# Kernel optimization log

Hardware: AMD Instinct MI355X
Metric: run time of the kernel (lower is better)

## Reference

```python
import jax, jax.numpy as jnp
import numpy as np

B, TT, C, H, T = 4, 4096, 1024, 16, 128
K = C // H  # head size (rk and v head sizes equal here)
HEAD_DIV = 8.0  # head_size_divisor
EPS = 1e-5  # GroupNorm eps
LAYER_ID, N_LAYER = 12, 24


def setup_inputs() -> dict:
    key = jax.random.key(0)
    ks = jax.random.split(key, 8)
    r01 = LAYER_ID / (N_LAYER - 1)
    r1a0 = 1.0 - LAYER_ID / N_LAYER
    ddd = (jnp.arange(C, dtype=jnp.float32) / C).reshape(1, 1, C)
    h = jnp.arange(H, dtype=jnp.float32)
    scale = 0.02
    return {
        "xq": jax.random.normal(ks[0], (B, TT, C), jnp.float32),
        "time_mix_k": ddd ** r1a0,
        "time_mix_v": ddd ** r1a0 + 0.3 * r01,
        "time_mix_r": ddd ** (0.5 * r1a0),
        "time_mix_g": ddd ** (0.5 * r1a0),
        "time_decay": -8.0 + 7.0 * (h / (H - 1)) ** (0.7 + 1.3 * r01),
        "time_faaaa": r01 * (1.0 - h / (H - 1)),
        "W_r": jax.random.normal(ks[1], (C, C), jnp.float32) * scale,
        "W_k": jax.random.normal(ks[2], (C, C), jnp.float32) * scale,
        "W_v": jax.random.normal(ks[3], (C, C), jnp.float32) * scale,
        "W_g": jax.random.normal(ks[4], (C, C), jnp.float32) * scale,
        "W_o": jax.random.normal(ks[5], (C, C), jnp.float32) * scale,
        "ln_w": jnp.ones((C,), jnp.float32),
        "ln_b": jnp.zeros((C,), jnp.float32),
    }


def reference(xq, time_mix_k, time_mix_v, time_mix_r, time_mix_g,
              time_decay, time_faaaa, W_r, W_k, W_v, W_g, W_o, ln_w, ln_b):
    x = xq
    B_, TT_, C_ = x.shape
    N = TT_ // T  # number of chunks
    # time shift: xx[:, t] = x[:, t-1], xx[:, 0] = 0
    xx = jnp.pad(x, ((0, 0), (1, 0), (0, 0)))[:, :-1]
    xr = x * time_mix_r + xx * (1 - time_mix_r)
    xk = x * time_mix_k + xx * (1 - time_mix_k)
    xv = x * time_mix_v + xx * (1 - time_mix_v)
    xg = x * time_mix_g + xx * (1 - time_mix_g)
    r = (xr @ W_r.T).reshape(B_, TT_, H, K).transpose(0, 2, 1, 3)  # (B,H,TT,K)
    k = (xk @ W_k.T).reshape(B_, TT_, H, K).transpose(0, 2, 1, 3)
    v = (xv @ W_v.T).reshape(B_, TT_, H, K).transpose(0, 2, 1, 3)
    g = jax.nn.silu(xg @ W_g.T)  # (B,TT,C)

    decay = jnp.exp(-jnp.exp(time_decay))  # (H,)
    u = time_faaaa  # (H,)
    ws = decay ** T  # per-chunk state decay (H,)
    i_idx = jnp.arange(T)
    wb = decay[:, None] ** i_idx                # (H,T): decay^i
    wk = decay[:, None] ** (T - 1 - i_idx)      # (H,T): decay^(T-1-j)
    diff = i_idx[:, None] - i_idx[None, :]      # i - j
    pw = decay[:, None, None] ** jnp.maximum(diff - 1, 0)
    # lower-triangular intra-chunk decay: decay^(i-j-1) for i>j, u on diag
    w_mat = jnp.where(diff > 0, pw, 0.0) + jnp.eye(T, dtype=x.dtype) * u[:, None, None]  # (H,T,T)

    # chunked layout: (N, B, H, T, K)
    rc = r.reshape(B_, H, N, T, K).transpose(2, 0, 1, 3, 4)
    kc = k.reshape(B_, H, N, T, K).transpose(2, 0, 1, 3, 4)
    vc = v.reshape(B_, H, N, T, K).transpose(2, 0, 1, 3, 4)
    s0 = jnp.zeros((B_, H, K, K), x.dtype)

    def step(s, chunk):
        rr, kk, vv = chunk
        att = jnp.einsum('bhik,bhjk->bhij', rr, kk) * w_mat
        out = att @ vv + jnp.einsum('bhik,bhkv->bhiv', rr, s) * wb[None, :, :, None]
        s_new = ws[None, :, None, None] * s + jnp.einsum(
            'bhjk,bhjv->bhkv', kk * wk[None, :, :, None], vv)
        return s_new, out

    _, xo = jax.lax.scan(step, s0, (rc, kc, vc))  # xo: (N,B,H,T,K)
    xo = xo.transpose(1, 0, 3, 2, 4).reshape(B_, TT_, H, K)

    # GroupNorm(H groups) over channels, applied to x / head_size_divisor
    y = xo / HEAD_DIV
    mu = y.mean(-1, keepdims=True)
    var = y.var(-1, keepdims=True)
    y = (y - mu) / jnp.sqrt(var + EPS)
    y = y * ln_w.reshape(H, K) + ln_b.reshape(H, K)
    y = y.reshape(B_, TT_, C_)
    return (y * g) @ W_o.T
```

## Files before the change

### kernel.cpp

```cpp
#include <hip/hip_runtime.h>
#include <hip/hip_bf16.h>
#include <stdint.h>

#define C_DIM 1024
#define H_DIM 16
#define K_DIM 64
#define T_CH 128
#define TT_DIM 4096
#define B_DIM 4
#define N_CH 32
#define M_ROWS 16384

typedef __attribute__((ext_vector_type(8))) __bf16 bf16x8;
typedef __attribute__((ext_vector_type(4))) float floatx4;

__device__ __forceinline__ float bf2f(ushort u) {
  union { uint32_t i; float f; } v; v.i = ((uint32_t)u) << 16; return v.f;
}
__device__ __forceinline__ ushort f2bf(float f) {
  union { float f; uint32_t i; } v; v.f = f;
  return (ushort)((v.i + 0x7fffu + ((v.i >> 16) & 1u)) >> 16);
}

#define GLOAD_LDS16(g, l)                                                     \
  __builtin_amdgcn_global_load_lds(                                           \
      (const __attribute__((address_space(1))) void*)(g),                     \
      (__attribute__((address_space(3))) void*)(l), 16, 0, 0)

__global__ __launch_bounds__(256) void mix_kernel(
    const float* __restrict__ x,
    const float* __restrict__ mk, const float* __restrict__ mv,
    const float* __restrict__ mr, const float* __restrict__ mg,
    ushort* __restrict__ xr, ushort* __restrict__ xk,
    ushort* __restrict__ xv, ushort* __restrict__ xg) {
  long idx = (long)blockIdx.x * 256 + threadIdx.x;
  long e = idx * 4;
  int c = (int)(e & (C_DIM - 1));
  long row = e >> 10;
  int t = (int)(row & (TT_DIM - 1));
  floatx4 xc = *(const floatx4*)(x + e);
  floatx4 xp = {0.f, 0.f, 0.f, 0.f};
  if (t != 0) xp = *(const floatx4*)(x + e - C_DIM);
  floatx4 d = xc - xp;
  floatx4 vk = *(const floatx4*)(mk + c);
  floatx4 vv = *(const floatx4*)(mv + c);
  floatx4 vr = *(const floatx4*)(mr + c);
  floatx4 vg = *(const floatx4*)(mg + c);
  floatx4 ok = xp + d * vk;
  floatx4 ov = xp + d * vv;
  floatx4 orr = xp + d * vr;
  floatx4 og = xp + d * vg;
  union { ushort u[4]; uint2 q; } pk;
#define ST(dst, val)                                                          \
  pk.u[0] = f2bf(val.x); pk.u[1] = f2bf(val.y);                               \
  pk.u[2] = f2bf(val.z); pk.u[3] = f2bf(val.w);                               \
  *(uint2*)((dst) + e) = pk.q;
  ST(xk, ok) ST(xv, ov) ST(xr, orr) ST(xg, og)
#undef ST
}

__global__ __launch_bounds__(256) void wconv_kernel(
    const float* __restrict__ w0, const float* __restrict__ w1,
    const float* __restrict__ w2, const float* __restrict__ w3,
    const float* __restrict__ w4, ushort* __restrict__ o) {
  long idx = (long)blockIdx.x * 256 + threadIdx.x;
  long e = idx * 4;
  int wi = (int)(e >> 20);
  long off = e & ((1L << 20) - 1);
  const float* src = wi == 0 ? w0 : wi == 1 ? w1 : wi == 2 ? w2 : wi == 3 ? w3 : w4;
  floatx4 vv = *(const floatx4*)(src + off);
  union { ushort u[4]; uint2 q; } pk;
  pk.u[0] = f2bf(vv.x); pk.u[1] = f2bf(vv.y);
  pk.u[2] = f2bf(vv.z); pk.u[3] = f2bf(vv.w);
  *(uint2*)(o + e) = pk.q;
}

#define BARX() __builtin_amdgcn_s_barrier()
#define VMW4() asm volatile("s_waitcnt vmcnt(4)" ::: "memory")
#define VMW0() asm volatile("s_waitcnt vmcnt(0)" ::: "memory")
#define LGKW() asm volatile("s_waitcnt lgkmcnt(0)" ::: "memory")

template <int EPI>
__global__ __launch_bounds__(512, 2) void gemm_bt(
    const ushort* __restrict__ A, const ushort* __restrict__ Bt,
    void* __restrict__ Cout) {
  __shared__ __align__(16) ushort smem[65536];
  const int tid = threadIdx.x;
  const int lane = tid & 63, w = tid >> 6;
  const int q = lane >> 4, l16 = lane & 15;
  const int wm = w >> 2, wn = w & 3;
  const int id = blockIdx.x;
  const int wg = (id & 7) * 32 + (id >> 3);
  const int bm = wg >> 2, bn = wg & 3;

  const int r8 = tid >> 3;
  const int c8 = ((tid & 7) ^ (r8 & 7)) * 8;
  const ushort* gA = A + (long)(bm * 256 + r8) * C_DIM + c8;
  const ushort* gB = Bt + (long)(bn * 256 + r8) * C_DIM + c8;

  const char* sB = (const char*)smem;
  const int arow = (wm * 128 + l16) * 128;
  const int brow = (wn * 64 + l16) * 128;
  const int swz = (l16 & 7) << 4;
  const int csv[2] = {(q << 4) ^ swz, ((4 + q) << 4) ^ swz};

  floatx4 acc[8][4] = {};
  bf16x8 af[4][2];
  bf16x8 bfv[4][2];

#define STAGE(ISA, sl, hh, tile)                                              \
  do {                                                                        \
    const ushort* g_ = (ISA ? gA : gB) + ((hh) * 131072 + (tile) * 64);       \
    ushort* l_ = smem + ((ISA ? 0 : 32768) + (sl) * 16384 + (hh) * 8192 +     \
                         w * 512);                                            \
    GLOAD_LDS16(g_, l_);                         \
    GLOAD_LDS16(g_ + 65536, l_ + 4096);                \
  } while (0)

#define READ_A(sl, qr)                                                        \
  do {                                                                        \
    _Pragma("unroll") for (int i_ = 0; i_ < 4; ++i_) {                        \
      af[i_][0] = *(const bf16x8*)(sB + (sl) * 32768 + arow + (qr) * 8192 +   \
                                   i_ * 2048 + csv[0]);                       \
      af[i_][1] = *(const bf16x8*)(sB + (sl) * 32768 + arow + (qr) * 8192 +   \
                                   i_ * 2048 + csv[1]);                       \
    }                                                                         \
  } while (0)

#define READ_B(sl, qc)                                                        \
  do {                                                                        \
    _Pragma("unroll") for (int j_ = 0; j_ < 2; ++j_) {                        \
      bfv[(qc) * 2 + j_][0] = *(const bf16x8*)(sB + 65536 + (sl) * 32768 +    \
                                               brow + (qc) * 4096 +           \
                                               j_ * 2048 + csv[0]);           \
      bfv[(qc) * 2 + j_][1] = *(const bf16x8*)(sB + 65536 + (sl) * 32768 +    \
                                               brow + (qc) * 4096 +           \
                                               j_ * 2048 + csv[1]);           \
    }                                                                         \
  } while (0)

#define MFMA_Q(qr, qc)                                                        \
  do {                                                                        \
    __builtin_amdgcn_s_setprio(1);                                            \
    _Pragma("unroll") for (int i_ = 0; i_ < 4; ++i_)                          \
        _Pragma("unroll") for (int j_ = 0; j_ < 2; ++j_) {                    \
      acc[(qr) * 4 + i_][(qc) * 2 + j_] =                                     \
          __builtin_amdgcn_mfma_f32_16x16x32_bf16(                            \
              af[i_][0], bfv[(qc) * 2 + j_][0],                               \
              acc[(qr) * 4 + i_][(qc) * 2 + j_], 0, 0, 0);                    \
      acc[(qr) * 4 + i_][(qc) * 2 + j_] =                                     \
          __builtin_amdgcn_mfma_f32_16x16x32_bf16(                            \
              af[i_][1], bfv[(qc) * 2 + j_][1],                               \
              acc[(qr) * 4 + i_][(qc) * 2 + j_], 0, 0, 0);                    \
    }                                                                         \
    __builtin_amdgcn_s_setprio(0);                                            \
  } while (0)

  STAGE(1, 0, 0, 0); STAGE(1, 0, 1, 0);
  STAGE(0, 0, 0, 0); STAGE(0, 0, 1, 0);
  STAGE(0, 1, 0, 1); STAGE(0, 1, 1, 1);
  VMW4();
  BARX();

#pragma unroll 1
  for (int i = 0; i < 7; ++i) {
    const int t1 = 2 * i + 1, tn0 = 2 * i + 2, tn1 = 2 * i + 3;
    READ_A(0, 0); READ_B(0, 0); STAGE(1, 1, 0, t1);
    BARX(); MFMA_Q(0, 0); LGKW(); BARX();
    READ_B(0, 1); STAGE(1, 1, 1, t1);
    BARX(); MFMA_Q(0, 1); LGKW(); BARX();
    READ_A(0, 1); STAGE(0, 0, 0, tn0);
    BARX(); MFMA_Q(1, 0); LGKW(); BARX();
    STAGE(0, 0, 1, tn0); VMW4();
    BARX(); MFMA_Q(1, 1); LGKW(); BARX();
    READ_A(1, 0); READ_B(1, 0); STAGE(1, 0, 0, tn0);
    BARX(); MFMA_Q(0, 0); LGKW(); BARX();
    READ_B(1, 1); STAGE(1, 0, 1, tn0);
    BARX(); MFMA_Q(0, 1); LGKW(); BARX();
    READ_A(1, 1); STAGE(0, 1, 0, tn1);
    BARX(); MFMA_Q(1, 0); LGKW(); BARX();
    STAGE(0, 1, 1, tn1); VMW4();
    BARX(); MFMA_Q(1, 1); LGKW(); BARX();
  }
  READ_A(0, 0); READ_B(0, 0); STAGE(1, 1, 0, 15);
  BARX(); MFMA_Q(0, 0); LGKW(); BARX();
  READ_B(0, 1); STAGE(1, 1, 1, 15);
  BARX(); MFMA_Q(0, 1); LGKW(); BARX();
  READ_A(0, 1);
  BARX(); MFMA_Q(1, 0); LGKW(); BARX();
  VMW0();
  BARX(); MFMA_Q(1, 1); LGKW(); BARX();
  READ_A(1, 0); READ_B(1, 0);
  BARX(); MFMA_Q(0, 0); LGKW(); BARX();
  READ_B(1, 1);
  BARX(); MFMA_Q(0, 1); LGKW(); BARX();
  READ_A(1, 1);
  BARX(); MFMA_Q(1, 0); LGKW(); BARX();
  BARX(); MFMA_Q(1, 1);

  const int row0 = bm * 256 + wm * 128 + q * 4;
  const int col0 = bn * 256 + wn * 64 + l16;
#pragma unroll
  for (int fi = 0; fi < 8; ++fi)
#pragma unroll
    for (int fj = 0; fj < 4; ++fj)
#pragma unroll
      for (int rg = 0; rg < 4; ++rg) {
        long off = (long)(row0 + fi * 16 + rg) * C_DIM + col0 + fj * 16;
        float val = acc[fi][fj][rg];
        if (EPI == 1) val = val / (1.f + expf(-val));
        if (EPI == 2)
          ((float*)Cout)[off] = val;
        else
          ((ushort*)Cout)[off] = f2bf(val);
      }
#undef STAGE
#undef READ_A
#undef READ_B
#undef MFMA_Q
}

__global__ __launch_bounds__(256) void chunk_state(
    const ushort* __restrict__ kB, const ushort* __restrict__ vB,
    const float* __restrict__ td, ushort* __restrict__ Zc) {
  __shared__ __align__(16) ushort vt_s[64 * 136];
  __shared__ __align__(16) ushort kwt_s[64 * 136];
  int blk = blockIdx.x;
  int bh = blk >> 5, n = blk & 31;
  int b = bh >> 4, h = bh & 15;
  int tid = threadIdx.x;
  int lane = tid & 63, w = tid >> 6;
  int q = lane >> 4, l16 = lane & 15;
  float etd = expf(td[h]);
  long cbase = ((long)b * TT_DIM + n * T_CH) * C_DIM + h * K_DIM;

#pragma unroll
  for (int it = 0; it < 4; it++) {
    int chunk = it * 256 + tid;
    int row = chunk >> 3;
    int cc = (chunk & 7) * 8;
    long ga = cbase + (long)row * C_DIM + cc;
    uint4 kv4 = *(const uint4*)(kB + ga);
    uint4 vv4 = *(const uint4*)(vB + ga);
    float wkj = expf(-(float)(T_CH - 1 - row) * etd);
    const ushort* kp = (const ushort*)&kv4;
    const ushort* vp = (const ushort*)&vv4;
#pragma unroll
    for (int e2 = 0; e2 < 8; e2++) {
      kwt_s[(cc + e2) * 136 + row] = f2bf(bf2f(kp[e2]) * wkj);
      vt_s[(cc + e2) * 136 + row] = vp[e2];
    }
  }
  __syncthreads();

  floatx4 accZ[4] = {};
#pragma unroll
  for (int js = 0; js < 128; js += 32) {
    bf16x8 av = *(const bf16x8*)&vt_s[(w * 16 + l16) * 136 + q * 8 + js];
    bf16x8 bk3[4];
#pragma unroll
    for (int kt = 0; kt < 4; kt++)
      bk3[kt] = *(const bf16x8*)&kwt_s[(kt * 16 + l16) * 136 + q * 8 + js];
#pragma unroll
    for (int kt = 0; kt < 4; kt++)
      accZ[kt] = __builtin_amdgcn_mfma_f32_16x16x32_bf16(av, bk3[kt], accZ[kt], 0, 0, 0);
  }
  long zbase = (long)blk * 4096;
#pragma unroll
  for (int kt = 0; kt < 4; kt++)
#pragma unroll
    for (int rg = 0; rg < 4; rg++)
      Zc[zbase + (w * 16 + q * 4 + rg) * 64 + kt * 16 + l16] = f2bf(accZ[kt][rg]);
}

__global__ __launch_bounds__(256) void state_scan(
    const ushort* __restrict__ Zc, const float* __restrict__ td,
    ushort* __restrict__ Sb) {
  long tg = (long)blockIdx.x * 256 + threadIdx.x;
  int bh = (int)(tg >> 12);
  int e = (int)(tg & 4095);
  int h = bh & 15;
  float wsf = expf(-128.f * expf(td[h]));
  float s = 0.f;
  long base = (long)bh * N_CH * 4096 + e;
#pragma unroll
  for (int n = 0; n < N_CH; n++) {
    Sb[base + n * 4096] = f2bf(s);
    s = wsf * s + bf2f(Zc[base + n * 4096]);
  }
}

__global__ __launch_bounds__(256) void chunk_out(
    const ushort* __restrict__ rB, const ushort* __restrict__ kB,
    const ushort* __restrict__ vB, const ushort* __restrict__ gBuf,
    const ushort* __restrict__ Sb,
    const float* __restrict__ td, const float* __restrict__ tf,
    const float* __restrict__ lnw, const float* __restrict__ lnb,
    ushort* __restrict__ gy) {
  __shared__ __align__(16) ushort rr_s[128 * 72];
  __shared__ __align__(16) ushort un_s[128 * 136];
  __shared__ __align__(16) ushort vt_s[64 * 136];
  __shared__ __align__(16) ushort z_s[64 * 72];

  int blk = blockIdx.x;
  int bh = blk >> 5, n = blk & 31;
  int b = bh >> 4, h = bh & 15;
  int tid = threadIdx.x;
  int lane = tid & 63, w = tid >> 6;
  int q = lane >> 4, l16 = lane & 15;

  float etd = expf(td[h]);
  float u = tf[h];
  long cbase = ((long)b * TT_DIM + n * T_CH) * C_DIM + h * K_DIM;

#pragma unroll
  for (int it = 0; it < 4; it++) {
    int chunk = it * 256 + tid;
    int row = chunk >> 3;
    int cc = (chunk & 7) * 8;
    long ga = cbase + (long)row * C_DIM + cc;
    *(uint4*)&rr_s[row * 72 + cc] = *(const uint4*)(rB + ga);
    *(uint4*)&un_s[row * 136 + cc] = *(const uint4*)(kB + ga);
    uint4 vv4 = *(const uint4*)(vB + ga);
    const ushort* vp = (const ushort*)&vv4;
#pragma unroll
    for (int e2 = 0; e2 < 8; e2++) vt_s[(cc + e2) * 136 + row] = vp[e2];
  }
  {
    long sbase = (long)blk * 4096;
    int v = tid >> 2, c0 = (tid & 3) * 16;
    *(uint4*)&z_s[v * 72 + c0] = *(const uint4*)(Sb + sbase + v * 64 + c0);
    *(uint4*)&z_s[v * 72 + c0 + 8] = *(const uint4*)(Sb + sbase + v * 64 + c0 + 8);
  }
  __syncthreads();

  floatx4 accA[4][4] = {};
  int ai0 = (w >> 1) * 64, aj0 = (w & 1) * 64;
#pragma unroll
  for (int ks = 0; ks < 64; ks += 32) {
    bf16x8 af[4], bk2[4];
#pragma unroll
    for (int i = 0; i < 4; i++)
      af[i] = *(const bf16x8*)&rr_s[(ai0 + i * 16 + l16) * 72 + q * 8 + ks];
#pragma unroll
    for (int j = 0; j < 4; j++)
      bk2[j] = *(const bf16x8*)&un_s[(aj0 + j * 16 + l16) * 136 + q * 8 + ks];
#pragma unroll
    for (int mi = 0; mi < 4; mi++)
#pragma unroll
      for (int nj = 0; nj < 4; nj++)
        accA[mi][nj] = __builtin_amdgcn_mfma_f32_16x16x32_bf16(
            af[mi], bk2[nj], accA[mi][nj], 0, 0, 0);
  }

  floatx4 accB[2][4] = {};
  int i0 = w * 32;
#pragma unroll
  for (int ks = 0; ks < 64; ks += 32) {
    bf16x8 af2[2], bz[4];
#pragma unroll
    for (int it2 = 0; it2 < 2; it2++)
      af2[it2] = *(const bf16x8*)&rr_s[(i0 + it2 * 16 + l16) * 72 + q * 8 + ks];
#pragma unroll
    for (int vt2 = 0; vt2 < 4; vt2++)
      bz[vt2] = *(const bf16x8*)&z_s[(vt2 * 16 + l16) * 72 + q * 8 + ks];
#pragma unroll
    for (int it2 = 0; it2 < 2; it2++)
#pragma unroll
      for (int vt2 = 0; vt2 < 4; vt2++)
        accB[it2][vt2] = __builtin_amdgcn_mfma_f32_16x16x32_bf16(
            af2[it2], bz[vt2], accB[it2][vt2], 0, 0, 0);
  }
  __syncthreads();

#pragma unroll
  for (int mi = 0; mi < 4; mi++)
#pragma unroll
    for (int nj = 0; nj < 4; nj++)
#pragma unroll
      for (int rg = 0; rg < 4; rg++) {
        int i = ai0 + mi * 16 + q * 4 + rg;
        int j = aj0 + nj * 16 + l16;
        float wv = 0.f;
        if (i > j) wv = expf(-(float)(i - j - 1) * etd);
        else if (i == j) wv = u;
        un_s[i * 136 + j] = f2bf(accA[mi][nj][rg] * wv);
      }
  __syncthreads();

  floatx4 accO[2][4] = {};
#pragma unroll
  for (int js = 0; js < 128; js += 32) {
    bf16x8 af3[2], bv[4];
#pragma unroll
    for (int it2 = 0; it2 < 2; it2++)
      af3[it2] = *(const bf16x8*)&un_s[(i0 + it2 * 16 + l16) * 136 + q * 8 + js];
#pragma unroll
    for (int vt2 = 0; vt2 < 4; vt2++)
      bv[vt2] = *(const bf16x8*)&vt_s[(vt2 * 16 + l16) * 136 + q * 8 + js];
#pragma unroll
    for (int it2 = 0; it2 < 2; it2++)
#pragma unroll
      for (int vt2 = 0; vt2 < 4; vt2++)
        accO[it2][vt2] = __builtin_amdgcn_mfma_f32_16x16x32_bf16(
            af3[it2], bv[vt2], accO[it2][vt2], 0, 0, 0);
  }

#pragma unroll
  for (int it2 = 0; it2 < 2; it2++)
#pragma unroll
    for (int rg = 0; rg < 4; rg++) {
      int i = i0 + it2 * 16 + q * 4 + rg;
      float wbi = expf(-(float)i * etd);
      float vals[4];
      float s1 = 0.f, s2 = 0.f;
#pragma unroll
      for (int vt2 = 0; vt2 < 4; vt2++) {
        float val = accO[it2][vt2][rg] + wbi * accB[it2][vt2][rg];
        vals[vt2] = val; s1 += val; s2 += val * val;
      }
#pragma unroll
      for (int mm = 1; mm < 16; mm <<= 1) {
        s1 += __shfl_xor(s1, mm, 64);
        s2 += __shfl_xor(s2, mm, 64);
      }
      float mu = s1 * (1.f / 64.f);
      float va = s2 * (1.f / 64.f) - mu * mu;
      float rinv = rsqrtf(va + 64.f * 1e-5f);
      long rowg = (long)b * TT_DIM + n * T_CH + i;
#pragma unroll
      for (int vt2 = 0; vt2 < 4; vt2++) {
        int c = h * K_DIM + vt2 * 16 + l16;
        float y = (vals[vt2] - mu) * rinv * lnw[c] + lnb[c];
        float gf = bf2f(gBuf[rowg * C_DIM + c]);
        gy[rowg * C_DIM + c] = f2bf(y * gf);
      }
    }
}

extern "C" void kernel_launch(void* const* d_in, const int* in_sizes, int n_in,
                              void* d_out, int out_size, void* d_ws,
                              size_t ws_size, hipStream_t stream) {
  const float* xq  = (const float*)d_in[0];
  const float* tmk = (const float*)d_in[1];
  const float* tmv = (const float*)d_in[2];
  const float* tmr = (const float*)d_in[3];
  const float* tmg = (const float*)d_in[4];
  const float* td  = (const float*)d_in[5];
  const float* tf  = (const float*)d_in[6];
  const float* Wr  = (const float*)d_in[7];
  const float* Wk  = (const float*)d_in[8];
  const float* Wv  = (const float*)d_in[9];
  const float* Wg  = (const float*)d_in[10];
  const float* Wo  = (const float*)d_in[11];
  const float* lnw = (const float*)d_in[12];
  const float* lnb = (const float*)d_in[13];

  char* ws = (char*)d_ws;
  const size_t BUF = (size_t)M_ROWS * C_DIM * 2;
  ushort* b0 = (ushort*)(ws + 0 * BUF);
  ushort* b1 = (ushort*)(ws + 1 * BUF);
  ushort* b2 = (ushort*)(ws + 2 * BUF);
  ushort* b3 = (ushort*)(ws + 3 * BUF);
  ushort* wcv = (ushort*)(ws + 4 * BUF);
  const ushort* wr_b = wcv;
  const ushort* wk_b = wcv + (1 << 20);
  const ushort* wv_b = wcv + 2 * (1 << 20);
  const ushort* wg_b = wcv + 3 * (1 << 20);
  const ushort* wo_b = wcv + 4 * (1 << 20);
  ushort* Zc = (ushort*)(ws + 4 * BUF + 5 * (2 << 20));
  ushort* Sb = Zc + (size_t)64 * N_CH * 4096;
  ushort* rbuf = (ushort*)d_out;

  mix_kernel<<<16384, 256, 0, stream>>>(xq, tmk, tmv, tmr, tmg, b0, b1, b2, b3);
  wconv_kernel<<<5120, 256, 0, stream>>>(Wr, Wk, Wv, Wg, Wo, wcv);

  gemm_bt<0><<<256, 512, 0, stream>>>(b0, wr_b, rbuf);
  gemm_bt<0><<<256, 512, 0, stream>>>(b1, wk_b, b0);
  gemm_bt<0><<<256, 512, 0, stream>>>(b2, wv_b, b1);
  gemm_bt<1><<<256, 512, 0, stream>>>(b3, wg_b, b2);

  chunk_state<<<2048, 256, 0, stream>>>(b0, b1, td, Zc);
  state_scan<<<1024, 256, 0, stream>>>(Zc, td, Sb);
  chunk_out<<<2048, 256, 0, stream>>>(rbuf, b0, b1, b2, Sb, td, tf, lnw, lnb, b3);

  gemm_bt<2><<<256, 512, 0, stream>>>(b3, wo_b, (float*)d_out);
}
```

Before: 434.9 us.

## Swizzle transposed LDS tiles and widen chunk_out to 512 threads

```diff
diff --git a/kernel.cpp b/kernel.cpp
--- a/kernel.cpp
+++ b/kernel.cpp
@@ -113,8 +113,8 @@
     const ushort* g_ = (ISA ? gA : gB) + ((hh) * 131072 + (tile) * 64);       \
     ushort* l_ = smem + ((ISA ? 0 : 32768) + (sl) * 16384 + (hh) * 8192 +     \
                          w * 512);                                            \
-    GLOAD_LDS16(g_, l_);                         \
-    GLOAD_LDS16(g_ + 65536, l_ + 4096);                \
+    GLOAD_LDS16(g_, l_);                                                      \
+    GLOAD_LDS16(g_ + 65536, l_ + 4096);                                       \
   } while (0)
 
 #define READ_A(sl, qr)                                                        \
@@ -245,10 +245,13 @@
     float wkj = expf(-(float)(T_CH - 1 - row) * etd);
     const ushort* kp = (const ushort*)&kv4;
     const ushort* vp = (const ushort*)&vv4;
+    int cb2 = row >> 3;
 #pragma unroll
     for (int e2 = 0; e2 < 8; e2++) {
-      kwt_s[(cc + e2) * 136 + row] = f2bf(bf2f(kp[e2]) * wkj);
-      vt_s[(cc + e2) * 136 + row] = vp[e2];
+      int vr = cc + e2;
+      int ph = vr * 136 + ((cb2 ^ ((vr >> 3) & 7)) << 3) + (row & 7);
+      kwt_s[ph] = f2bf(bf2f(kp[e2]) * wkj);
+      vt_s[ph] = vp[e2];
     }
   }
   __syncthreads();
@@ -256,11 +259,15 @@
   floatx4 accZ[4] = {};
 #pragma unroll
   for (int js = 0; js < 128; js += 32) {
-    bf16x8 av = *(const bf16x8*)&vt_s[(w * 16 + l16) * 136 + q * 8 + js];
+    int cb = q + (js >> 3);
+    int vrA = w * 16 + l16;
+    bf16x8 av = *(const bf16x8*)&vt_s[vrA * 136 + ((cb ^ ((vrA >> 3) & 7)) << 3)];
     bf16x8 bk3[4];
 #pragma unroll
-    for (int kt = 0; kt < 4; kt++)
-      bk3[kt] = *(const bf16x8*)&kwt_s[(kt * 16 + l16) * 136 + q * 8 + js];
+    for (int kt = 0; kt < 4; kt++) {
+      int vrB = kt * 16 + l16;
+      bk3[kt] = *(const bf16x8*)&kwt_s[vrB * 136 + ((cb ^ ((vrB >> 3) & 7)) << 3)];
+    }
 #pragma unroll
     for (int kt = 0; kt < 4; kt++)
       accZ[kt] = __builtin_amdgcn_mfma_f32_16x16x32_bf16(av, bk3[kt], accZ[kt], 0, 0, 0);
@@ -290,7 +297,7 @@
   }
 }
 
-__global__ __launch_bounds__(256) void chunk_out(
+__global__ __launch_bounds__(512, 4) void chunk_out(
     const ushort* __restrict__ rB, const ushort* __restrict__ kB,
     const ushort* __restrict__ vB, const ushort* __restrict__ gBuf,
     const ushort* __restrict__ Sb,
@@ -301,6 +308,7 @@
   __shared__ __align__(16) ushort un_s[128 * 136];
   __shared__ __align__(16) ushort vt_s[64 * 136];
   __shared__ __align__(16) ushort z_s[64 * 72];
+  __shared__ float pw_s[128];
 
   int blk = blockIdx.x;
   int bh = blk >> 5, n = blk & 31;
@@ -313,9 +321,11 @@
   float u = tf[h];
   long cbase = ((long)b * TT_DIM + n * T_CH) * C_DIM + h * K_DIM;
 
-#pragma unroll
-  for (int it = 0; it < 4; it++) {
-    int chunk = it * 256 + tid;
+  if (tid < 128) pw_s[tid] = expf(-(float)tid * etd);
+
+#pragma unroll
+  for (int it = 0; it < 2; it++) {
+    int chunk = it * 512 + tid;
     int row = chunk >> 3;
     int cc = (chunk & 7) * 8;
     long ga = cbase + (long)row * C_DIM + cc;
@@ -323,119 +333,115 @@
     *(uint4*)&un_s[row * 136 + cc] = *(const uint4*)(kB + ga);
     uint4 vv4 = *(const uint4*)(vB + ga);
     const ushort* vp = (const ushort*)&vv4;
-#pragma unroll
-    for (int e2 = 0; e2 < 8; e2++) vt_s[(cc + e2) * 136 + row] = vp[e2];
+    int cb2 = row >> 3;
+#pragma unroll
+    for (int e2 = 0; e2 < 8; e2++) {
+      int vr = cc + e2;
+      vt_s[vr * 136 + ((cb2 ^ ((vr >> 3) & 7)) << 3) + (row & 7)] = vp[e2];
+    }
   }
   {
     long sbase = (long)blk * 4096;
-    int v = tid >> 2, c0 = (tid & 3) * 16;
+    int v = tid >> 3, c0 = (tid & 7) * 8;
     *(uint4*)&z_s[v * 72 + c0] = *(const uint4*)(Sb + sbase + v * 64 + c0);
-    *(uint4*)&z_s[v * 72 + c0 + 8] = *(const uint4*)(Sb + sbase + v * 64 + c0 + 8);
   }
   __syncthreads();
 
-  floatx4 accA[4][4] = {};
-  int ai0 = (w >> 1) * 64, aj0 = (w & 1) * 64;
+  int ar0 = (w >> 1) * 32, ac0 = (w & 1) * 64;
+  floatx4 accA[2][4] = {};
 #pragma unroll
   for (int ks = 0; ks < 64; ks += 32) {
-    bf16x8 af[4], bk2[4];
-#pragma unroll
-    for (int i = 0; i < 4; i++)
-      af[i] = *(const bf16x8*)&rr_s[(ai0 + i * 16 + l16) * 72 + q * 8 + ks];
+    bf16x8 af[2], bk2[4];
+#pragma unroll
+    for (int i = 0; i < 2; i++)
+      af[i] = *(const bf16x8*)&rr_s[(ar0 + i * 16 + l16) * 72 + q * 8 + ks];
 #pragma unroll
     for (int j = 0; j < 4; j++)
-      bk2[j] = *(const bf16x8*)&un_s[(aj0 + j * 16 + l16) * 136 + q * 8 + ks];
-#pragma unroll
-    for (int mi = 0; mi < 4; mi++)
+      bk2[j] = *(const bf16x8*)&un_s[(ac0 + j * 16 + l16) * 136 + q * 8 + ks];
+#pragma unroll
+    for (int mi = 0; mi < 2; mi++)
 #pragma unroll
       for (int nj = 0; nj < 4; nj++)
         accA[mi][nj] = __builtin_amdgcn_mfma_f32_16x16x32_bf16(
             af[mi], bk2[nj], accA[mi][nj], 0, 0, 0);
   }
 
-  floatx4 accB[2][4] = {};
-  int i0 = w * 32;
+  int i0 = w * 16;
+  floatx4 accB[4] = {};
 #pragma unroll
   for (int ks = 0; ks < 64; ks += 32) {
-    bf16x8 af2[2], bz[4];
-#pragma unroll
-    for (int it2 = 0; it2 < 2; it2++)
-      af2[it2] = *(const bf16x8*)&rr_s[(i0 + it2 * 16 + l16) * 72 + q * 8 + ks];
+    bf16x8 af2 = *(const bf16x8*)&rr_s[(i0 + l16) * 72 + q * 8 + ks];
+    bf16x8 bz[4];
 #pragma unroll
     for (int vt2 = 0; vt2 < 4; vt2++)
       bz[vt2] = *(const bf16x8*)&z_s[(vt2 * 16 + l16) * 72 + q * 8 + ks];
 #pragma unroll
-    for (int it2 = 0; it2 < 2; it2++)
-#pragma unroll
-      for (int vt2 = 0; vt2 < 4; vt2++)
-        accB[it2][vt2] = __builtin_amdgcn_mfma_f32_16x16x32_bf16(
-            af2[it2], bz[vt2], accB[it2][vt2], 0, 0, 0);
+    for (int vt2 = 0; vt2 < 4; vt2++)
+      accB[vt2] = __builtin_amdgcn_mfma_f32_16x16x32_bf16(
+          af2, bz[vt2], accB[vt2], 0, 0, 0);
   }
   __syncthreads();
 
 #pragma unroll
-  for (int mi = 0; mi < 4; mi++)
+  for (int mi = 0; mi < 2; mi++)
 #pragma unroll
     for (int nj = 0; nj < 4; nj++)
 #pragma unroll
       for (int rg = 0; rg < 4; rg++) {
-        int i = ai0 + mi * 16 + q * 4 + rg;
-        int j = aj0 + nj * 16 + l16;
+        int i = ar0 + mi * 16 + q * 4 + rg;
+        int j = ac0 + nj * 16 + l16;
         float wv = 0.f;
-        if (i > j) wv = expf(-(float)(i - j - 1) * etd);
+        if (i > j) wv = pw_s[i - j - 1];
         else if (i == j) wv = u;
         un_s[i * 136 + j] = f2bf(accA[mi][nj][rg] * wv);
       }
   __syncthreads();
 
-  floatx4 accO[2][4] = {};
+  floatx4 accO[4] = {};
 #pragma unroll
   for (int js = 0; js < 128; js += 32) {
-    bf16x8 af3[2], bv[4];
-#pragma unroll
-    for (int it2 = 0; it2 < 2; it2++)
-      af3[it2] = *(const bf16x8*)&un_s[(i0 + it2 * 16 + l16) * 136 + q * 8 + js];
+    bf16x8 af3 = *(const bf16x8*)&un_s[(i0 + l16) * 136 + q * 8 + js];
+    int cb = q + (js >> 3);
+    bf16x8 bv[4];
+#pragma unroll
+    for (int vt2 = 0; vt2 < 4; vt2++) {
+      int vr = vt2 * 16 + l16;
+      bv[vt2] = *(const bf16x8*)&vt_s[vr * 136 + ((cb ^ ((vr >> 3) & 7)) << 3)];
+    }
 #pragma unroll
     for (int vt2 = 0; vt2 < 4; vt2++)
-      bv[vt2] = *(const bf16x8*)&vt_s[(vt2 * 16 + l16) * 136 + q * 8 + js];
-#pragma unroll
-    for (int it2 = 0; it2 < 2; it2++)
-#pragma unroll
-      for (int vt2 = 0; vt2 < 4; vt2++)
-        accO[it2][vt2] = __builtin_amdgcn_mfma_f32_16x16x32_bf16(
-            af3[it2], bv[vt2], accO[it2][vt2], 0, 0, 0);
-  }
-
-#pragma unroll
-  for (int it2 = 0; it2 < 2; it2++)
-#pragma unroll
-    for (int rg = 0; rg < 4; rg++) {
-      int i = i0 + it2 * 16 + q * 4 + rg;
-      float wbi = expf(-(float)i * etd);
-      float vals[4];
-      float s1 = 0.f, s2 = 0.f;
-#pragma unroll
-      for (int vt2 = 0; vt2 < 4; vt2++) {
-        float val = accO[it2][vt2][rg] + wbi * accB[it2][vt2][rg];
-        vals[vt2] = val; s1 += val; s2 += val * val;
-      }
-#pragma unroll
-      for (int mm = 1; mm < 16; mm <<= 1) {
-        s1 += __shfl_xor(s1, mm, 64);
-        s2 += __shfl_xor(s2, mm, 64);
-      }
-      float mu = s1 * (1.f / 64.f);
-      float va = s2 * (1.f / 64.f) - mu * mu;
-      float rinv = rsqrtf(va + 64.f * 1e-5f);
-      long rowg = (long)b * TT_DIM + n * T_CH + i;
-#pragma unroll
-      for (int vt2 = 0; vt2 < 4; vt2++) {
-        int c = h * K_DIM + vt2 * 16 + l16;
-        float y = (vals[vt2] - mu) * rinv * lnw[c] + lnb[c];
-        float gf = bf2f(gBuf[rowg * C_DIM + c]);
-        gy[rowg * C_DIM + c] = f2bf(y * gf);
-      }
-    }
+      accO[vt2] = __builtin_amdgcn_mfma_f32_16x16x32_bf16(
+          af3, bv[vt2], accO[vt2], 0, 0, 0);
+  }
+
+#pragma unroll
+  for (int rg = 0; rg < 4; rg++) {
+    int i = i0 + q * 4 + rg;
+    float wbi = pw_s[i];
+    float vals[4];
+    float s1 = 0.f, s2 = 0.f;
+#pragma unroll
+    for (int vt2 = 0; vt2 < 4; vt2++) {
+      float val = accO[vt2][rg] + wbi * accB[vt2][rg];
+      vals[vt2] = val; s1 += val; s2 += val * val;
+    }
+#pragma unroll
+    for (int mm = 1; mm < 16; mm <<= 1) {
+      s1 += __shfl_xor(s1, mm, 64);
+      s2 += __shfl_xor(s2, mm, 64);
+    }
+    float mu = s1 * (1.f / 64.f);
+    float va = s2 * (1.f / 64.f) - mu * mu;
+    float rinv = rsqrtf(va + 64.f * 1e-5f);
+    long rowg = (long)b * TT_DIM + n * T_CH + i;
+#pragma unroll
+    for (int vt2 = 0; vt2 < 4; vt2++) {
+      int c = h * K_DIM + vt2 * 16 + l16;
+      float y = (vals[vt2] - mu) * rinv * lnw[c] + lnb[c];
+      float gf = bf2f(gBuf[rowg * C_DIM + c]);
+      gy[rowg * C_DIM + c] = f2bf(y * gf);
+    }
+  }
 }
 
 extern "C" void kernel_launch(void* const* d_in, const int* in_sizes, int n_in,
@@ -482,7 +488,7 @@
 
   chunk_state<<<2048, 256, 0, stream>>>(b0, b1, td, Zc);
   state_scan<<<1024, 256, 0, stream>>>(Zc, td, Sb);
-  chunk_out<<<2048, 256, 0, stream>>>(rbuf, b0, b1, b2, Sb, td, tf, lnw, lnb, b3);
+  chunk_out<<<2048, 512, 0, stream>>>(rbuf, b0, b1, b2, Sb, td, tf, lnw, lnb, b3);
 
   gemm_bt<2><<<256, 512, 0, stream>>>(b3, wo_b, (float*)d_out);
 }
```

New measurement: 414.5 us. 4.7% less time.
